# Kernel tuning notes

Measured on AMD Instinct MI355X. Metric: run time of the kernel, lower is better.

The kernel has to match this reference:

```python
import jax, jax.numpy as jnp
import numpy as np

B, N, D, LAT, EC = 1024, 256, 64, 128, 32


def setup_inputs() -> dict:
    key = jax.random.key(0)
    ks = jax.random.split(key, 8)
    s = lambda d: 1.0 / np.sqrt(d)
    return {
        "local_data": jax.random.normal(ks[0], (B, D), jnp.float32),
        "neighbor_data": jax.random.normal(ks[1], (B, N, D), jnp.float32),
        "Wc": jax.random.normal(ks[2], (D, EC), jnp.float32) * s(D),
        "bc": jnp.zeros((EC,), jnp.float32),
        "Wf": jax.random.normal(ks[3], (D, LAT), jnp.float32) * s(D),
        "bf": jnp.zeros((LAT,), jnp.float32),
        "Wa": jax.random.normal(ks[4], (3 * EC, LAT), jnp.float32) * s(3 * EC),
        "ba": jnp.zeros((LAT,), jnp.float32),
        "Wl": jax.random.normal(ks[5], (LAT, LAT), jnp.float32) * s(LAT),
        "bl": jnp.zeros((LAT,), jnp.float32),
    }


def reference(local_data, neighbor_data, Wc, bc, Wf, bf, Wa, ba, Wl, bl):
    # per-neighbor feature encoder: [B,N,LAT]
    enc_feature = jax.nn.relu(jnp.einsum("bnd,dk->bnk", neighbor_data, Wf) + bf)
    # per-neighbor communication encoder: [B,N,EC]
    enc_comm = jax.nn.relu(jnp.einsum("bnd,dk->bnk", neighbor_data, Wc) + bc)
    # self communication embedding: [B,EC]
    enc_comm_self = jax.nn.relu(local_data @ Wc + bc)
    # broadcast self and neighbor-mean to [B,N,EC]
    self_rep = jnp.broadcast_to(enc_comm_self[:, None, :], enc_comm.shape)
    mean_rep = jnp.broadcast_to(enc_comm.mean(axis=1, keepdims=True), enc_comm.shape)
    cat = jnp.concatenate([self_rep, enc_comm, mean_rep], axis=-1)  # [B,N,3*EC]
    # attention: linear then softmax over neighbor axis (dim=-2)
    att = jax.nn.softmax(jnp.einsum("bnc,ck->bnk", cat, Wa) + ba, axis=1)  # [B,N,LAT]
    # attention-weighted sum over neighbors: [B,LAT]
    aggregated = jnp.einsum("bnk,bnk->bk", att, enc_feature)
    # later layer
    return jax.nn.relu(aggregated @ Wl + bl)
```

## Files before the change

kernel.cpp:

```cpp
#include <hip/hip_runtime.h>

#define NB    256
#define DIN   64
#define LATD  128
#define ECD   32

typedef __attribute__((ext_vector_type(8))) __bf16 bf16x8;
typedef __attribute__((ext_vector_type(4))) float f32x4;

#define XS_STRIDE 72
#define EC_STRIDE 40
#define WA_STRIDE 40

#define WS_WC 0
#define WS_WF (32 * 72)
#define WS_WA (32 * 72 + 128 * 72)

#define MFMA(a, b, c) __builtin_amdgcn_mfma_f32_16x16x32_bf16((a), (b), (c), 0, 0, 0)

__device__ __forceinline__ unsigned short f2bf(float f) {
    unsigned u = __builtin_bit_cast(unsigned, f);
    u += 0x7fffu + ((u >> 16) & 1u);
    return (unsigned short)(u >> 16);
}

__device__ __forceinline__ bf16x8 pack8(float4 a, float4 b) {
    union { unsigned short u[8]; bf16x8 v; } r;
    r.u[0] = f2bf(a.x); r.u[1] = f2bf(a.y); r.u[2] = f2bf(a.z); r.u[3] = f2bf(a.w);
    r.u[4] = f2bf(b.x); r.u[5] = f2bf(b.y); r.u[6] = f2bf(b.z); r.u[7] = f2bf(b.w);
    return r.v;
}

__global__ __launch_bounds__(256) void prep_kernel(
    const float* __restrict__ Wc, const float* __restrict__ Wf,
    const float* __restrict__ Wa, unsigned short* __restrict__ ws)
{
    int t = blockIdx.x * blockDim.x + threadIdx.x;
    int stride = gridDim.x * blockDim.x;
    for (int i = t; i < 32 * 64; i += stride) {
        int n = i >> 6, k = i & 63;
        ws[WS_WC + n * XS_STRIDE + k] = f2bf(Wc[k * ECD + n]);
    }
    for (int i = t; i < 128 * 64; i += stride) {
        int n = i >> 6, k = i & 63;
        ws[WS_WF + n * XS_STRIDE + k] = f2bf(Wf[k * LATD + n]);
    }
    for (int i = t; i < 128 * 32; i += stride) {
        int n = i >> 5, k = i & 31;
        ws[WS_WA + n * WA_STRIDE + k] = f2bf(Wa[(ECD + k) * LATD + n]);
    }
}

__global__ __launch_bounds__(256, 4) void arm_main(
    const float* __restrict__ xg,
    const float* __restrict__ bcv,
    const float* __restrict__ bfv,
    const float* __restrict__ wl,
    const float* __restrict__ blv,
    const unsigned short* __restrict__ ws,
    float* __restrict__ out)
{
    __shared__ unsigned short ecs[NB * EC_STRIDE];
    __shared__ float aggnum[4][LATD];
    __shared__ float aggden[4][LATD];
    __shared__ float aggfull[LATD];
    __shared__ float wlpart[2][LATD];

    const int b    = blockIdx.x;
    const int tid  = threadIdx.x;
    const int lane = tid & 63;
    const int w    = tid >> 6;
    const int l15  = lane & 15;
    const int q    = lane >> 4;

    const float* xb = xg + (size_t)b * NB * DIN;
    bf16x8 xfrag[4][2];
    #pragma unroll
    for (int t = 0; t < 4; ++t) {
        const float* p = xb + (w * 64 + t * 16 + l15) * DIN + q * 8;
        float4 a0 = *reinterpret_cast<const float4*>(p);
        float4 a1 = *reinterpret_cast<const float4*>(p + 4);
        xfrag[t][0] = pack8(a0, a1);
        float4 a2 = *reinterpret_cast<const float4*>(p + 32);
        float4 a3 = *reinterpret_cast<const float4*>(p + 36);
        xfrag[t][1] = pack8(a2, a3);
    }

    {
        bf16x8 wfrag[2][2];
        #pragma unroll
        for (int ks = 0; ks < 2; ++ks)
            #pragma unroll
            for (int nb = 0; nb < 2; ++nb)
                wfrag[ks][nb] = *reinterpret_cast<const bf16x8*>(
                    &ws[WS_WC + (nb * 16 + l15) * XS_STRIDE + ks * 32 + q * 8]);

        float bc0 = bcv[l15], bc1 = bcv[16 + l15];
        #pragma unroll
        for (int t = 0; t < 4; ++t) {
            int rowA = w * 64 + t * 16;
            f32x4 a0 = {0.f, 0.f, 0.f, 0.f}, a1 = {0.f, 0.f, 0.f, 0.f};
            #pragma unroll
            for (int ks = 0; ks < 2; ++ks) {
                a0 = MFMA(xfrag[t][ks], wfrag[ks][0], a0);
                a1 = MFMA(xfrag[t][ks], wfrag[ks][1], a1);
            }
            #pragma unroll
            for (int r = 0; r < 4; ++r) {
                int row = rowA + q * 4 + r;
                ecs[row * EC_STRIDE + l15]      = f2bf(fmaxf(a0[r] + bc0, 0.f));
                ecs[row * EC_STRIDE + 16 + l15] = f2bf(fmaxf(a1[r] + bc1, 0.f));
            }
        }
    }

    bf16x8 ecfrag[4];
    #pragma unroll
    for (int t = 0; t < 4; ++t)
        ecfrag[t] = *reinterpret_cast<const bf16x8*>(
            &ecs[(w * 64 + t * 16 + l15) * EC_STRIDE + q * 8]);

    for (int g = 0; g < 8; ++g) {
        bf16x8 wf0 = *reinterpret_cast<const bf16x8*>(
            &ws[WS_WF + (g * 16 + l15) * XS_STRIDE + q * 8]);
        bf16x8 wf1 = *reinterpret_cast<const bf16x8*>(
            &ws[WS_WF + (g * 16 + l15) * XS_STRIDE + 32 + q * 8]);
        bf16x8 wag = *reinterpret_cast<const bf16x8*>(
            &ws[WS_WA + (g * 16 + l15) * WA_STRIDE + q * 8]);

        f32x4 ef[4], lg[4];
        #pragma unroll
        for (int t = 0; t < 4; ++t) {
            f32x4 z = {0.f, 0.f, 0.f, 0.f};
            z = MFMA(xfrag[t][0], wf0, z);
            ef[t] = MFMA(xfrag[t][1], wf1, z);
            f32x4 z2 = {0.f, 0.f, 0.f, 0.f};
            lg[t] = MFMA(ecfrag[t], wag, z2);
        }
        float bfl = bfv[g * 16 + l15];
        float num = 0.f, den = 0.f;
        #pragma unroll
        for (int t = 0; t < 4; ++t)
            #pragma unroll
            for (int r = 0; r < 4; ++r) {
                float e = fmaxf(ef[t][r] + bfl, 0.f);
                float p = exp2f(lg[t][r] * 1.44269504f);
                num += p * e;
                den += p;
            }
        num += __shfl_xor(num, 16, 64); num += __shfl_xor(num, 32, 64);
        den += __shfl_xor(den, 16, 64); den += __shfl_xor(den, 32, 64);
        if (lane < 16) {
            aggnum[w][g * 16 + lane] = num;
            aggden[w][g * 16 + lane] = den;
        }
    }
    __syncthreads();

    if (tid < 128) {
        float num = aggnum[0][tid] + aggnum[1][tid] + aggnum[2][tid] + aggnum[3][tid];
        float den = aggden[0][tid] + aggden[1][tid] + aggden[2][tid] + aggden[3][tid];
        aggfull[tid] = num / den;
    }
    __syncthreads();

    {
        int c = tid & 127, h = tid >> 7;
        float acc = 0.f;
        #pragma unroll 16
        for (int k = h * 64; k < h * 64 + 64; ++k)
            acc += aggfull[k] * wl[k * LATD + c];
        wlpart[h][c] = acc;
    }
    __syncthreads();
    if (tid < 128)
        out[(size_t)b * LATD + tid] =
            fmaxf(wlpart[0][tid] + wlpart[1][tid] + blv[tid], 0.f);
}

extern "C" void kernel_launch(void* const* d_in, const int* in_sizes, int n_in,
                              void* d_out, int out_size, void* d_ws, size_t ws_size,
                              hipStream_t stream)
{
    const float* xg  = (const float*)d_in[1];
    const float* wc  = (const float*)d_in[2];
    const float* bc_ = (const float*)d_in[3];
    const float* wf  = (const float*)d_in[4];
    const float* bf_ = (const float*)d_in[5];
    const float* wa  = (const float*)d_in[6];
    const float* wl  = (const float*)d_in[8];
    const float* bl_ = (const float*)d_in[9];
    unsigned short* wsp = (unsigned short*)d_ws;
    float* out = (float*)d_out;

    prep_kernel<<<8, 256, 0, stream>>>(wc, wf, wa, wsp);
    arm_main<<<1024, 256, 0, stream>>>(xg, bc_, bf_, wl, bl_, wsp, out);
}
```

Baseline: 128.8 us.

## Use packed bf16 converts, fold log2e into Wa, transpose Wl for vector loads

Swaps the software bf16 rounding for the packed hardware convert builtin when it is available. Folds the log2(e) scale into the pre-converted Wa weights so the exp2 needs no multiply. Hoists the bf bias loads out of the fully unrolled group loop. Transposes Wl in the prep kernel so each thread in the final layer reads contiguous float4s instead of strided scalars. This adds a larger prep kernel with more blocks, and the unrolling raises register pressure.

```diff
diff --git a/kernel.cpp b/kernel.cpp
--- a/kernel.cpp
+++ b/kernel.cpp
@@ -6,15 +6,20 @@
 #define ECD   32
 
 typedef __attribute__((ext_vector_type(8))) __bf16 bf16x8;
+typedef __attribute__((ext_vector_type(2))) __bf16 bf16x2;
 typedef __attribute__((ext_vector_type(4))) float f32x4;
 
 #define XS_STRIDE 72
 #define EC_STRIDE 40
 #define WA_STRIDE 40
 
-#define WS_WC 0
-#define WS_WF (32 * 72)
-#define WS_WA (32 * 72 + 128 * 72)
+#define WS_WC  0
+#define WS_WF  (32 * 72)
+#define WS_WA  (32 * 72 + 128 * 72)
+#define WS_END (32 * 72 + 128 * 72 + 128 * 40)
+#define WS_WLT_BYTES 33280
+
+#define LOG2E 1.44269504f
 
 #define MFMA(a, b, c) __builtin_amdgcn_mfma_f32_16x16x32_bf16((a), (b), (c), 0, 0, 0)
 
@@ -24,16 +29,27 @@
     return (unsigned short)(u >> 16);
 }
 
+__device__ __forceinline__ bf16x2 cvt2(float a, float b) {
+#if defined(__has_builtin) && __has_builtin(__builtin_amdgcn_cvt_pk_bf16_f32)
+    return __builtin_amdgcn_cvt_pk_bf16_f32(a, b);
+#else
+    union { unsigned short u[2]; bf16x2 v; } r;
+    r.u[0] = f2bf(a); r.u[1] = f2bf(b);
+    return r.v;
+#endif
+}
+
 __device__ __forceinline__ bf16x8 pack8(float4 a, float4 b) {
-    union { unsigned short u[8]; bf16x8 v; } r;
-    r.u[0] = f2bf(a.x); r.u[1] = f2bf(a.y); r.u[2] = f2bf(a.z); r.u[3] = f2bf(a.w);
-    r.u[4] = f2bf(b.x); r.u[5] = f2bf(b.y); r.u[6] = f2bf(b.z); r.u[7] = f2bf(b.w);
+    union { bf16x2 h[4]; bf16x8 v; } r;
+    r.h[0] = cvt2(a.x, a.y); r.h[1] = cvt2(a.z, a.w);
+    r.h[2] = cvt2(b.x, b.y); r.h[3] = cvt2(b.z, b.w);
     return r.v;
 }
 
 __global__ __launch_bounds__(256) void prep_kernel(
     const float* __restrict__ Wc, const float* __restrict__ Wf,
-    const float* __restrict__ Wa, unsigned short* __restrict__ ws)
+    const float* __restrict__ Wa, const float* __restrict__ Wl,
+    unsigned short* __restrict__ ws)
 {
     int t = blockIdx.x * blockDim.x + threadIdx.x;
     int stride = gridDim.x * blockDim.x;
@@ -47,7 +63,12 @@
     }
     for (int i = t; i < 128 * 32; i += stride) {
         int n = i >> 5, k = i & 31;
-        ws[WS_WA + n * WA_STRIDE + k] = f2bf(Wa[(ECD + k) * LATD + n]);
+        ws[WS_WA + n * WA_STRIDE + k] = f2bf(Wa[(ECD + k) * LATD + n] * LOG2E);
+    }
+    float* wlt = reinterpret_cast<float*>(reinterpret_cast<char*>(ws) + WS_WLT_BYTES);
+    for (int i = t; i < 128 * 128; i += stride) {
+        int c = i >> 7, k = i & 127;
+        wlt[c * 128 + k] = Wl[k * LATD + c];
     }
 }
 
@@ -55,7 +76,6 @@
     const float* __restrict__ xg,
     const float* __restrict__ bcv,
     const float* __restrict__ bfv,
-    const float* __restrict__ wl,
     const float* __restrict__ blv,
     const unsigned short* __restrict__ ws,
     float* __restrict__ out)
@@ -80,9 +100,9 @@
         const float* p = xb + (w * 64 + t * 16 + l15) * DIN + q * 8;
         float4 a0 = *reinterpret_cast<const float4*>(p);
         float4 a1 = *reinterpret_cast<const float4*>(p + 4);
-        xfrag[t][0] = pack8(a0, a1);
         float4 a2 = *reinterpret_cast<const float4*>(p + 32);
         float4 a3 = *reinterpret_cast<const float4*>(p + 36);
+        xfrag[t][0] = pack8(a0, a1);
         xfrag[t][1] = pack8(a2, a3);
     }
 
@@ -108,8 +128,10 @@
             #pragma unroll
             for (int r = 0; r < 4; ++r) {
                 int row = rowA + q * 4 + r;
-                ecs[row * EC_STRIDE + l15]      = f2bf(fmaxf(a0[r] + bc0, 0.f));
-                ecs[row * EC_STRIDE + 16 + l15] = f2bf(fmaxf(a1[r] + bc1, 0.f));
+                union { bf16x2 v; unsigned short u[2]; } pr;
+                pr.v = cvt2(fmaxf(a0[r] + bc0, 0.f), fmaxf(a1[r] + bc1, 0.f));
+                ecs[row * EC_STRIDE + l15]      = pr.u[0];
+                ecs[row * EC_STRIDE + 16 + l15] = pr.u[1];
             }
         }
     }
@@ -120,6 +142,11 @@
         ecfrag[t] = *reinterpret_cast<const bf16x8*>(
             &ecs[(w * 64 + t * 16 + l15) * EC_STRIDE + q * 8]);
 
+    float bfl8[8];
+    #pragma unroll
+    for (int g = 0; g < 8; ++g) bfl8[g] = bfv[g * 16 + l15];
+
+    #pragma unroll
     for (int g = 0; g < 8; ++g) {
         bf16x8 wf0 = *reinterpret_cast<const bf16x8*>(
             &ws[WS_WF + (g * 16 + l15) * XS_STRIDE + q * 8]);
@@ -137,14 +164,14 @@
             f32x4 z2 = {0.f, 0.f, 0.f, 0.f};
             lg[t] = MFMA(ecfrag[t], wag, z2);
         }
-        float bfl = bfv[g * 16 + l15];
+        float bfl = bfl8[g];
         float num = 0.f, den = 0.f;
         #pragma unroll
         for (int t = 0; t < 4; ++t)
             #pragma unroll
             for (int r = 0; r < 4; ++r) {
                 float e = fmaxf(ef[t][r] + bfl, 0.f);
-                float p = exp2f(lg[t][r] * 1.44269504f);
+                float p = exp2f(lg[t][r]);
                 num += p * e;
                 den += p;
             }
@@ -165,11 +192,18 @@
     __syncthreads();
 
     {
+        const float* wlt = reinterpret_cast<const float*>(
+            reinterpret_cast<const char*>(ws) + WS_WLT_BYTES);
         int c = tid & 127, h = tid >> 7;
+        const float* wr = wlt + c * 128 + h * 64;
         float acc = 0.f;
-        #pragma unroll 16
-        for (int k = h * 64; k < h * 64 + 64; ++k)
-            acc += aggfull[k] * wl[k * LATD + c];
+        #pragma unroll
+        for (int j = 0; j < 16; ++j) {
+            float4 v = *reinterpret_cast<const float4*>(wr + j * 4);
+            int k = h * 64 + j * 4;
+            acc += aggfull[k] * v.x + aggfull[k + 1] * v.y +
+                   aggfull[k + 2] * v.z + aggfull[k + 3] * v.w;
+        }
         wlpart[h][c] = acc;
     }
     __syncthreads();
@@ -193,6 +227,6 @@
     unsigned short* wsp = (unsigned short*)d_ws;
     float* out = (float*)d_out;
 
-    prep_kernel<<<8, 256, 0, stream>>>(wc, wf, wa, wsp);
-    arm_main<<<1024, 256, 0, stream>>>(xg, bc_, bf_, wl, bl_, wsp, out);
-}
+    prep_kernel<<<16, 256, 0, stream>>>(wc, wf, wa, wl, wsp);
+    arm_main<<<1024, 256, 0, stream>>>(xg, bc_, bf_, bl_, wsp, out);
+}
```

Result: slower. 133.8 us (+3.9%).
